# Performance work log

Measured on AMD Instinct MI355X. Metric: run time of the kernel, lower is better.

## Reference

```python
import jax, jax.numpy as jnp
import numpy as np

KERNELS = (7, 9, 11)   # kernel_sizes, dilation=1 each
HEADS_PER = 2          # num_head // len(kernel_sizes)
HEAD_DIM = 32          # dim // num_head
DIM = 192


def _win_idx(L, K):
    # NATTEN non-causal window start: centered, clamped to stay in-bounds.
    starts = jnp.clip(jnp.arange(L) - K // 2, 0, L - K)
    return starts[:, None] + jnp.arange(K)[None, :]  # [L, K]


def _na2d(q, k, v, K):
    # q,k,v: [B, h, H, W, D]; q pre-scaled. Neighborhood attention, kernel KxK.
    B, h, H, W, D = q.shape
    ih = _win_idx(H, K)  # [H, K]
    iw = _win_idx(W, K)  # [W, K]
    kr = k[:, :, ih]     # [B, h, H, Kh, W, D]  rows gathered once
    # loop over the Kw kernel taps (small fixed structural loop)
    attn = jnp.stack(
        [jnp.einsum('bnijd,bnikjd->bnijk', q, kr[:, :, :, :, iw[:, kw], :])
         for kw in range(K)], axis=-1)                 # [B,h,H,W,Kh,Kw]
    attn = jax.nn.softmax(attn.reshape(B, h, H, W, K * K), axis=-1)
    attn = attn.reshape(B, h, H, W, K, K)
    vr = v[:, :, ih]     # [B, h, H, Kh, W, D]
    y = jnp.zeros_like(q)
    for kw in range(K):
        y = y + jnp.einsum('bnijk,bnikjd->bnijd',
                           attn[..., kw], vr[:, :, :, :, iw[:, kw], :])
    return y             # [B, h, H, W, D]


def _forward(x, w_qkv, b_qkv, w_proj, b_proj):
    B, H, W, C = x.shape
    qkv = x @ w_qkv + b_qkv                      # [B,H,W,3*DIM]
    scale = HEAD_DIM ** -0.5
    outs = []
    off = 0
    for K in KERNELS:
        ch = 3 * HEADS_PER * HEAD_DIM            # 192 per scale
        xi = qkv[..., off:off + ch]
        off += ch
        r = xi.reshape(B, H, W, 3, HEADS_PER, HEAD_DIM)
        q = jnp.transpose(r[:, :, :, 0], (0, 3, 1, 2, 4)) * scale
        k = jnp.transpose(r[:, :, :, 1], (0, 3, 1, 2, 4))
        v = jnp.transpose(r[:, :, :, 2], (0, 3, 1, 2, 4))
        y = _na2d(q, k, v, K)                    # [B,h,H,W,D]
        outs.append(jnp.transpose(y, (0, 2, 3, 1, 4)).reshape(B, H, W, HEADS_PER * HEAD_DIM))
    out = jnp.concatenate(outs, axis=-1)         # [B,H,W,DIM]
    return out @ w_proj + b_proj


def setup_inputs() -> dict:
    key = jax.random.key(0)
    ks = jax.random.split(key, 4)
    x = jax.random.normal(ks[0], (4, 96, 96, DIM), jnp.float32)
    w_qkv = jax.random.normal(ks[1], (DIM, 3 * DIM), jnp.float32) * 0.02
    b_qkv = jnp.zeros((3 * DIM,), jnp.float32)
    w_proj = jax.random.normal(ks[2], (DIM, DIM), jnp.float32) * 0.02
    b_proj = jnp.zeros((DIM,), jnp.float32)
    return {'x': x, 'w_qkv': w_qkv, 'b_qkv': b_qkv, 'w_proj': w_proj, 'b_proj': b_proj}


def reference(x, w_qkv, b_qkv, w_proj, b_proj):
    return _forward(x, w_qkv, b_qkv, w_proj, b_proj)
```

## Files before the change

kernel.cpp:

```cpp
#include <hip/hip_runtime.h>
#include <cstddef>

constexpr int B_ = 4, H_ = 96, W_ = 96, C_ = 192, QKVC = 576;
constexpr int NPIX = B_ * H_ * W_;
constexpr float C2 = 0.25503486208385085f;

typedef __attribute__((ext_vector_type(8))) short bf16x8;
typedef __attribute__((ext_vector_type(4))) float f32x4;
typedef unsigned short ushort_t;

__device__ __forceinline__ unsigned short f2bf(float f) {
    unsigned int u = __builtin_bit_cast(unsigned int, f);
    u += 0x7fffu + ((u >> 16) & 1u);
    return (unsigned short)(u >> 16);
}
__device__ __forceinline__ float bf2f(unsigned short h) {
    unsigned int u = ((unsigned int)h) << 16;
    return __builtin_bit_cast(float, u);
}
__device__ __forceinline__ unsigned int pack2(unsigned short a, unsigned short b) {
    return (unsigned int)a | ((unsigned int)b << 16);
}
__device__ __forceinline__ float fexp2(float x) {
#if __has_builtin(__builtin_amdgcn_exp2f)
    return __builtin_amdgcn_exp2f(x);
#else
    return __expf(x * 0.6931471805599453f);
#endif
}

__global__ __launch_bounds__(256) void convert_x_kernel(
    const float* __restrict__ x, ushort_t* __restrict__ xh, int n4)
{
    int i = blockIdx.x * 256 + threadIdx.x;
    if (i >= n4) return;
    float4 v = ((const float4*)x)[i];
    uint2 p;
    p.x = pack2(f2bf(v.x), f2bf(v.y));
    p.y = pack2(f2bf(v.z), f2bf(v.w));
    ((uint2*)xh)[i] = p;
}

__global__ __launch_bounds__(256) void convert_w_kernel(
    const float* __restrict__ w_qkv, const float* __restrict__ w_proj,
    ushort_t* __restrict__ wqt, ushort_t* __restrict__ wpt_h,
    ushort_t* __restrict__ wpt_l)
{
    int idx = blockIdx.x * 256 + threadIdx.x;
    if (idx < 576 * 192) {
        int n = idx / 192, k = idx - n * 192;
        wqt[idx] = f2bf(w_qkv[(size_t)k * 576 + n]);
    } else {
        int i2 = idx - 576 * 192;
        if (i2 < 192 * 192) {
            int n = i2 / 192, k = i2 - n * 192;
            float v = w_proj[(size_t)k * 192 + n];
            unsigned short h = f2bf(v);
            wpt_h[i2] = h;
            wpt_l[i2] = f2bf(v - bf2f(h));
        }
    }
}

template<bool BSPLIT, bool OUTBF, bool VT, int NT>
__global__ __launch_bounds__(256) void gemm_mfma2_kernel(
    const ushort_t* __restrict__ A,
    const ushort_t* __restrict__ Bt_h, const ushort_t* __restrict__ Bt_l,
    const float* __restrict__ bias, void* __restrict__ Cout,
    ushort_t* __restrict__ vTout, int M, int N, int K)
{
    constexpr int NPB = BSPLIT ? 2 : 1;
    constexpr int NI = NT / 32;
    __shared__ __align__(16) ushort_t As[8 * 64 * 8];
    __shared__ __align__(16) ushort_t Bs[NPB][8 * NT * 8];

    const int tid = threadIdx.x;
    const int lane = tid & 63;
    const int w = tid >> 6;
    const int wm = (w & 1) * 32;
    const int wn = (w >> 1) * (NT / 2);
    const int fm = lane & 15;
    const int fq = lane >> 4;

    const int phys = blockIdx.x;
    const int bid = (phys & 7) * (int)(gridDim.x >> 3) + (phys >> 3);
    const int ntiles = N / NT;
    const int m0 = (bid / ntiles) * 64;
    const int n0 = (bid % ntiles) * NT;

    f32x4 acc[2][NI];
    #pragma unroll
    for (int mi = 0; mi < 2; ++mi)
        #pragma unroll
        for (int ni = 0; ni < NI; ++ni)
            acc[mi][ni] = (f32x4){0.f, 0.f, 0.f, 0.f};

    for (int k0 = 0; k0 < K; k0 += 64) {
        __syncthreads();
        #pragma unroll
        for (int it = 0; it < 2; ++it) {
            int idx = it * 256 + tid;
            int m = idx >> 3, kc = idx & 7;
            uint4 v = *(const uint4*)(A + (size_t)(m0 + m) * K + k0 + kc * 8);
            *(uint4*)(&As[0] + (kc * 64 + (m ^ kc)) * 8) = v;
        }
        #pragma unroll
        for (int it = 0; it < NI; ++it) {
            int idx = it * 256 + tid;
            int n = idx >> 3, kc = idx & 7;
            int phys_g = kc * NT + (n ^ kc);
            *(uint4*)(&Bs[0][0] + phys_g * 8) =
                *(const uint4*)(Bt_h + (size_t)(n0 + n) * K + k0 + kc * 8);
            if constexpr (BSPLIT)
                *(uint4*)(&Bs[NPB - 1][0] + phys_g * 8) =
                    *(const uint4*)(Bt_l + (size_t)(n0 + n) * K + k0 + kc * 8);
        }
        __syncthreads();

        #pragma unroll
        for (int kt2 = 0; kt2 < 2; ++kt2) {
            const int kc = kt2 * 4 + fq;
            bf16x8 ah[2], bh[NI];
            #pragma unroll
            for (int mi = 0; mi < 2; ++mi)
                ah[mi] = *(const bf16x8*)(&As[0] + (kc * 64 + ((wm + mi * 16 + fm) ^ kc)) * 8);
            #pragma unroll
            for (int ni = 0; ni < NI; ++ni)
                bh[ni] = *(const bf16x8*)(&Bs[0][0] + (kc * NT + ((wn + ni * 16 + fm) ^ kc)) * 8);
            #pragma unroll
            for (int mi = 0; mi < 2; ++mi)
                #pragma unroll
                for (int ni = 0; ni < NI; ++ni)
                    acc[mi][ni] = __builtin_amdgcn_mfma_f32_16x16x32_bf16(
                        ah[mi], bh[ni], acc[mi][ni], 0, 0, 0);
            if constexpr (BSPLIT) {
                bf16x8 bl[NI];
                #pragma unroll
                for (int ni = 0; ni < NI; ++ni)
                    bl[ni] = *(const bf16x8*)(&Bs[NPB - 1][0] + (kc * NT + ((wn + ni * 16 + fm) ^ kc)) * 8);
                #pragma unroll
                for (int mi = 0; mi < 2; ++mi)
                    #pragma unroll
                    for (int ni = 0; ni < NI; ++ni)
                        acc[mi][ni] = __builtin_amdgcn_mfma_f32_16x16x32_bf16(
                            ah[mi], bl[ni], acc[mi][ni], 0, 0, 0);
            }
        }
    }

    #pragma unroll
    for (int ni = 0; ni < NI; ++ni) {
        const int lcol = wn + ni * 16 + fm;
        const int col = n0 + lcol;
        const float bv = bias[col];
        const int vl = lcol - 128;
        #pragma unroll
        for (int mi = 0; mi < 2; ++mi) {
            const int rbase = m0 + wm + mi * 16 + fq * 4;
            if constexpr (VT) {
                if (vl >= 0) {
                    int bb = rbase / 9216;
                    int rem = rbase - bb * 9216;
                    int ii = rem / 96;
                    int jj = rem - ii * 96;
                    int hh = vl >> 5, dd = vl & 31;
                    unsigned long long pk =
                          (unsigned long long)f2bf(acc[mi][ni][0] + bv)
                        | ((unsigned long long)f2bf(acc[mi][ni][1] + bv) << 16)
                        | ((unsigned long long)f2bf(acc[mi][ni][2] + bv) << 32)
                        | ((unsigned long long)f2bf(acc[mi][ni][3] + bv) << 48);
                    *(unsigned long long*)(vTout
                        + ((size_t)((bb * 96 + ii) * 6) + (n0 / 192) * 2 + hh) * 3072
                        + (size_t)dd * 96 + jj) = pk;
                    continue;
                }
            }
            #pragma unroll
            for (int r = 0; r < 4; ++r) {
                float val = acc[mi][ni][r] + bv;
                if constexpr (OUTBF)
                    ((ushort_t*)Cout)[(size_t)(rbase + r) * N + col] = f2bf(val);
                else
                    ((float*)Cout)[(size_t)(rbase + r) * N + col] = val;
            }
        }
    }
}

__global__ __launch_bounds__(384, 5) void na2d_kernel(
    const ushort_t* __restrict__ qkv, const ushort_t* __restrict__ vT,
    ushort_t* __restrict__ attn)
{
    __shared__ ushort_t Kb[2][96 * 40];
    __shared__ ushort_t Vtb[2][32 * 104];
    __shared__ ushort_t Pb[6][16 * 40];

    int phys = blockIdx.x;
    int idx = (phys & 7) * 288 + (phys >> 3);

    const int g = idx % 3; idx /= 3;
    const int h = idx & 1; idx >>= 1;
    const int i = idx % 96;
    const int b = idx / 96;

    const int K = 7 + 2 * g, cc = K >> 1;
    int si = i - cc; if (si < 0) si = 0; if (si > H_ - K) si = H_ - K;

    const int tid = threadIdx.x;
    const int w = tid >> 6, lane = tid & 63;
    const int fm = lane & 15, fq = lane >> 4;
    const int pixbase = w * 16;

    int cb = (pixbase - cc) & ~7;
    if (cb < 0) cb = 0; if (cb > 64) cb = 64;
    const int col0 = cb + fm, col1 = cb + 16 + fm;

    float bm0[4], bm1[4];
    #pragma unroll
    for (int r = 0; r < 4; ++r) {
        int jj = pixbase + fq * 4 + r - cc;
        if (jj < 0) jj = 0; if (jj > W_ - K) jj = W_ - K;
        bm0[r] = ((unsigned)(col0 - jj) < (unsigned)K) ? 0.f : -1e30f;
        bm1[r] = ((unsigned)(col1 - jj) < (unsigned)K) ? 0.f : -1e30f;
    }

    const size_t rowstride = (size_t)W_ * QKVC;
    const bf16x8 qfrag = *(const bf16x8*)(
        qkv + (size_t)(b * H_ + i) * rowstride + (size_t)(pixbase + fm) * QKVC
        + g * 192 + h * 32 + fq * 8);

    const int scol = tid >> 2, sch = tid & 3;
    const size_t kgoff = (size_t)scol * QKVC + g * 192 + 64 + h * 32 + sch * 8;
    const int klds = scol * 40 + ((sch ^ (scol & 3)) << 3);
    const int vd = tid / 12, vc8 = tid - vd * 12;
    const int vlds = vd * 104 + vc8 * 8;
    const size_t vslice = ((size_t)((b * H_ + si) * 6) + g * 2 + h) * 3072;

    f32x4 y0 = {0.f, 0.f, 0.f, 0.f}, y1 = {0.f, 0.f, 0.f, 0.f};
    float lacc[4] = {0.f, 0.f, 0.f, 0.f};

    uint4 kv = *(const uint4*)(qkv + (size_t)(b * H_ + si) * rowstride + kgoff);
    uint4 vv = *(const uint4*)(vT + vslice + (size_t)tid * 8);

    for (int t = 0; t < K; ++t) {
        *(uint4*)&Kb[t & 1][klds] = kv;
        *(uint4*)&Vtb[t & 1][vlds] = vv;
        if (t + 1 < K) {
            kv = *(const uint4*)(qkv + (size_t)(b * H_ + si + t + 1) * rowstride + kgoff);
            vv = *(const uint4*)(vT + vslice + (size_t)(t + 1) * 18432 + (size_t)tid * 8);
        }
        __syncthreads();

        bf16x8 kf0 = *(const bf16x8*)&Kb[t & 1][col0 * 40 + ((fq ^ (col0 & 3)) << 3)];
        bf16x8 kf1 = *(const bf16x8*)&Kb[t & 1][col1 * 40 + ((fq ^ (col1 & 3)) << 3)];
        f32x4 s0 = __builtin_amdgcn_mfma_f32_16x16x32_bf16(
            qfrag, kf0, (f32x4){0.f, 0.f, 0.f, 0.f}, 0, 0, 0);
        f32x4 s1 = __builtin_amdgcn_mfma_f32_16x16x32_bf16(
            qfrag, kf1, (f32x4){0.f, 0.f, 0.f, 0.f}, 0, 0, 0);

        #pragma unroll
        for (int r = 0; r < 4; ++r) {
            float e0 = fexp2(fmaf(s0[r], C2, bm0[r]));
            float e1 = fexp2(fmaf(s1[r], C2, bm1[r]));
            unsigned short p0 = f2bf(e0), p1 = f2bf(e1);
            lacc[r] += bf2f(p0) + bf2f(p1);
            const int m = fq * 4 + r;
            Pb[w][m * 40 + (((fm >> 3) ^ (m & 3)) << 3) + (fm & 7)] = p0;
            Pb[w][m * 40 + ((((fm >> 3) + 2) ^ (m & 3)) << 3) + (fm & 7)] = p1;
        }

        bf16x8 pf = *(const bf16x8*)&Pb[w][fm * 40 + ((fq ^ (fm & 3)) << 3)];
        bf16x8 vf0 = *(const bf16x8*)&Vtb[t & 1][fm * 104 + cb + fq * 8];
        bf16x8 vf1 = *(const bf16x8*)&Vtb[t & 1][(16 + fm) * 104 + cb + fq * 8];
        y0 = __builtin_amdgcn_mfma_f32_16x16x32_bf16(pf, vf0, y0, 0, 0, 0);
        y1 = __builtin_amdgcn_mfma_f32_16x16x32_bf16(pf, vf1, y1, 0, 0, 0);
    }

    #pragma unroll
    for (int r = 0; r < 4; ++r) {
        float l = lacc[r];
        l += __shfl_xor(l, 1); l += __shfl_xor(l, 2);
        l += __shfl_xor(l, 4); l += __shfl_xor(l, 8);
        const float inv = 1.f / l;
        const int j = pixbase + fq * 4 + r;
        const size_t o = (size_t)((b * H_ + i) * W_ + j) * C_ + g * 64 + h * 32 + fm;
        attn[o]      = f2bf(y0[r] * inv);
        attn[o + 16] = f2bf(y1[r] * inv);
    }
}

extern "C" void kernel_launch(void* const* d_in, const int* in_sizes, int n_in,
                              void* d_out, int out_size, void* d_ws, size_t ws_size,
                              hipStream_t stream)
{
    const float* x      = (const float*)d_in[0];
    const float* w_qkv  = (const float*)d_in[1];
    const float* b_qkv  = (const float*)d_in[2];
    const float* w_proj = (const float*)d_in[3];
    const float* b_proj = (const float*)d_in[4];
    float* out = (float*)d_out;

    char* ws = (char*)d_ws;
    ushort_t* qkvh  = (ushort_t*)ws;
    char*     reg1  = ws + (size_t)NPIX * QKVC * 2;
    ushort_t* xh    = (ushort_t*)reg1;
    ushort_t* attn  = (ushort_t*)reg1;
    char*     wbase = reg1 + (size_t)NPIX * C_ * 2;
    ushort_t* wqt   = (ushort_t*)wbase;
    ushort_t* wpt_h = (ushort_t*)(wbase + 576 * 192 * 2);
    ushort_t* wpt_l = (ushort_t*)(wbase + 576 * 192 * 2 + 192 * 192 * 2);
    ushort_t* vT    = (ushort_t*)(wbase + 576 * 192 * 2 + 2 * 192 * 192 * 2);

    convert_x_kernel<<<(NPIX * C_ / 4 + 255) / 256, 256, 0, stream>>>(
        x, xh, NPIX * C_ / 4);
    convert_w_kernel<<<(576 * 192 + 192 * 192 + 255) / 256, 256, 0, stream>>>(
        w_qkv, w_proj, wqt, wpt_h, wpt_l);

    gemm_mfma2_kernel<false, true, true, 192><<<(NPIX / 64) * (QKVC / 192), 256, 0, stream>>>(
        xh, wqt, nullptr, b_qkv, qkvh, vT, NPIX, QKVC, C_);

    na2d_kernel<<<2304, 384, 0, stream>>>(qkvh, vT, attn);

    gemm_mfma2_kernel<true, false, false, 96><<<(NPIX / 64) * (C_ / 96), 256, 0, stream>>>(
        attn, wpt_h, wpt_l, b_proj, out, nullptr, NPIX, C_, C_);
}
```

Baseline: 161.1 us.

## Drop LDS staging in NA2D kernel; load K/V fragments directly into registers

The neighborhood-attention kernel no longer stages K, V and the probability tile through shared memory with __syncthreads. Each lane now loads its MFMA K and V fragments straight from global memory with register double-buffering. Swapping the QK^T operand order leaves the score tile in the layout needed for the PV MFMA, so P is packed in registers. Blocks shrink from 384 to 128 threads with three times as many blocks, which removes LDS traffic and barriers but adds redundant, less coalesced global loads that now rely on cache.

```diff
diff --git a/kernel.cpp b/kernel.cpp
--- a/kernel.cpp
+++ b/kernel.cpp
@@ -187,21 +187,18 @@
     }
 }
 
-__global__ __launch_bounds__(384, 5) void na2d_kernel(
+__global__ __launch_bounds__(128, 4) void na2d_kernel(
     const ushort_t* __restrict__ qkv, const ushort_t* __restrict__ vT,
     ushort_t* __restrict__ attn)
 {
-    __shared__ ushort_t Kb[2][96 * 40];
-    __shared__ ushort_t Vtb[2][32 * 104];
-    __shared__ ushort_t Pb[6][16 * 40];
-
     int phys = blockIdx.x;
-    int idx = (phys & 7) * 288 + (phys >> 3);
-
-    const int g = idx % 3; idx /= 3;
-    const int h = idx & 1; idx >>= 1;
-    const int i = idx % 96;
-    const int b = idx / 96;
+    int idx = (phys & 7) * 864 + (phys >> 3);
+
+    const int c2 = idx % 3; idx /= 3;
+    const int g  = idx % 3; idx /= 3;
+    const int h  = idx & 1; idx >>= 1;
+    const int i  = idx % 96;
+    const int b  = idx / 96;
 
     const int K = 7 + 2 * g, cc = K >> 1;
     int si = i - cc; if (si < 0) si = 0; if (si > H_ - K) si = H_ - K;
@@ -209,78 +206,84 @@
     const int tid = threadIdx.x;
     const int w = tid >> 6, lane = tid & 63;
     const int fm = lane & 15, fq = lane >> 4;
-    const int pixbase = w * 16;
+    const int pixbase = (c2 * 2 + w) * 16;
 
     int cb = (pixbase - cc) & ~7;
     if (cb < 0) cb = 0; if (cb > 64) cb = 64;
-    const int col0 = cb + fm, col1 = cb + 16 + fm;
-
-    float bm0[4], bm1[4];
+
+    const int jlane = pixbase + fm;
+    int sjl = jlane - cc; if (sjl < 0) sjl = 0; if (sjl > W_ - K) sjl = W_ - K;
+    float b0[4], b1[4];
     #pragma unroll
     for (int r = 0; r < 4; ++r) {
-        int jj = pixbase + fq * 4 + r - cc;
-        if (jj < 0) jj = 0; if (jj > W_ - K) jj = W_ - K;
-        bm0[r] = ((unsigned)(col0 - jj) < (unsigned)K) ? 0.f : -1e30f;
-        bm1[r] = ((unsigned)(col1 - jj) < (unsigned)K) ? 0.f : -1e30f;
+        b0[r] = ((unsigned)(cb + fq * 4 + r - sjl)      < (unsigned)K) ? 0.f : -1e30f;
+        b1[r] = ((unsigned)(cb + 16 + fq * 4 + r - sjl) < (unsigned)K) ? 0.f : -1e30f;
     }
 
     const size_t rowstride = (size_t)W_ * QKVC;
     const bf16x8 qfrag = *(const bf16x8*)(
-        qkv + (size_t)(b * H_ + i) * rowstride + (size_t)(pixbase + fm) * QKVC
+        qkv + (size_t)(b * H_ + i) * rowstride + (size_t)jlane * QKVC
         + g * 192 + h * 32 + fq * 8);
 
-    const int scol = tid >> 2, sch = tid & 3;
-    const size_t kgoff = (size_t)scol * QKVC + g * 192 + 64 + h * 32 + sch * 8;
-    const int klds = scol * 40 + ((sch ^ (scol & 3)) << 3);
-    const int vd = tid / 12, vc8 = tid - vd * 12;
-    const int vlds = vd * 104 + vc8 * 8;
+    const ushort_t* kp0 = qkv + (size_t)(b * H_ + si) * rowstride
+        + (size_t)(cb + fm) * QKVC + g * 192 + 64 + h * 32 + fq * 8;
+    const ushort_t* kp1 = kp0 + (size_t)16 * QKVC;
     const size_t vslice = ((size_t)((b * H_ + si) * 6) + g * 2 + h) * 3072;
+    const ushort_t* vp = vT + vslice + (size_t)fm * 96 + cb + fq * 4;
 
     f32x4 y0 = {0.f, 0.f, 0.f, 0.f}, y1 = {0.f, 0.f, 0.f, 0.f};
-    float lacc[4] = {0.f, 0.f, 0.f, 0.f};
-
-    uint4 kv = *(const uint4*)(qkv + (size_t)(b * H_ + si) * rowstride + kgoff);
-    uint4 vv = *(const uint4*)(vT + vslice + (size_t)tid * 8);
+    float lsum = 0.f;
+
+    bf16x8 kf0 = *(const bf16x8*)kp0;
+    bf16x8 kf1 = *(const bf16x8*)kp1;
+    uint2 va = *(const uint2*)(vp);
+    uint2 vb = *(const uint2*)(vp + 16);
+    uint2 vc = *(const uint2*)(vp + 1536);
+    uint2 vd = *(const uint2*)(vp + 1552);
 
     for (int t = 0; t < K; ++t) {
-        *(uint4*)&Kb[t & 1][klds] = kv;
-        *(uint4*)&Vtb[t & 1][vlds] = vv;
+        const bf16x8 ck0 = kf0, ck1 = kf1;
+        const bf16x8 cv0 = __builtin_bit_cast(bf16x8, (uint4){va.x, va.y, vb.x, vb.y});
+        const bf16x8 cv1 = __builtin_bit_cast(bf16x8, (uint4){vc.x, vc.y, vd.x, vd.y});
         if (t + 1 < K) {
-            kv = *(const uint4*)(qkv + (size_t)(b * H_ + si + t + 1) * rowstride + kgoff);
-            vv = *(const uint4*)(vT + vslice + (size_t)(t + 1) * 18432 + (size_t)tid * 8);
-        }
-        __syncthreads();
-
-        bf16x8 kf0 = *(const bf16x8*)&Kb[t & 1][col0 * 40 + ((fq ^ (col0 & 3)) << 3)];
-        bf16x8 kf1 = *(const bf16x8*)&Kb[t & 1][col1 * 40 + ((fq ^ (col1 & 3)) << 3)];
+            kp0 += rowstride; kp1 += rowstride; vp += 18432;
+            kf0 = *(const bf16x8*)kp0;
+            kf1 = *(const bf16x8*)kp1;
+            va = *(const uint2*)(vp);
+            vb = *(const uint2*)(vp + 16);
+            vc = *(const uint2*)(vp + 1536);
+            vd = *(const uint2*)(vp + 1552);
+        }
+
         f32x4 s0 = __builtin_amdgcn_mfma_f32_16x16x32_bf16(
-            qfrag, kf0, (f32x4){0.f, 0.f, 0.f, 0.f}, 0, 0, 0);
+            ck0, qfrag, (f32x4){0.f, 0.f, 0.f, 0.f}, 0, 0, 0);
         f32x4 s1 = __builtin_amdgcn_mfma_f32_16x16x32_bf16(
-            qfrag, kf1, (f32x4){0.f, 0.f, 0.f, 0.f}, 0, 0, 0);
-
-        #pragma unroll
-        for (int r = 0; r < 4; ++r) {
-            float e0 = fexp2(fmaf(s0[r], C2, bm0[r]));
-            float e1 = fexp2(fmaf(s1[r], C2, bm1[r]));
-            unsigned short p0 = f2bf(e0), p1 = f2bf(e1);
-            lacc[r] += bf2f(p0) + bf2f(p1);
-            const int m = fq * 4 + r;
-            Pb[w][m * 40 + (((fm >> 3) ^ (m & 3)) << 3) + (fm & 7)] = p0;
-            Pb[w][m * 40 + ((((fm >> 3) + 2) ^ (m & 3)) << 3) + (fm & 7)] = p1;
-        }
-
-        bf16x8 pf = *(const bf16x8*)&Pb[w][fm * 40 + ((fq ^ (fm & 3)) << 3)];
-        bf16x8 vf0 = *(const bf16x8*)&Vtb[t & 1][fm * 104 + cb + fq * 8];
-        bf16x8 vf1 = *(const bf16x8*)&Vtb[t & 1][(16 + fm) * 104 + cb + fq * 8];
-        y0 = __builtin_amdgcn_mfma_f32_16x16x32_bf16(pf, vf0, y0, 0, 0, 0);
-        y1 = __builtin_amdgcn_mfma_f32_16x16x32_bf16(pf, vf1, y1, 0, 0, 0);
-    }
+            ck1, qfrag, (f32x4){0.f, 0.f, 0.f, 0.f}, 0, 0, 0);
+
+        unsigned short p00 = f2bf(fexp2(fmaf(s0[0], C2, b0[0])));
+        unsigned short p01 = f2bf(fexp2(fmaf(s0[1], C2, b0[1])));
+        unsigned short p02 = f2bf(fexp2(fmaf(s0[2], C2, b0[2])));
+        unsigned short p03 = f2bf(fexp2(fmaf(s0[3], C2, b0[3])));
+        unsigned short p10 = f2bf(fexp2(fmaf(s1[0], C2, b1[0])));
+        unsigned short p11 = f2bf(fexp2(fmaf(s1[1], C2, b1[1])));
+        unsigned short p12 = f2bf(fexp2(fmaf(s1[2], C2, b1[2])));
+        unsigned short p13 = f2bf(fexp2(fmaf(s1[3], C2, b1[3])));
+        lsum += (bf2f(p00) + bf2f(p01)) + (bf2f(p02) + bf2f(p03))
+              + (bf2f(p10) + bf2f(p11)) + (bf2f(p12) + bf2f(p13));
+        const bf16x8 pa = __builtin_bit_cast(bf16x8, (uint4){
+            pack2(p00, p01), pack2(p02, p03),
+            pack2(p10, p11), pack2(p12, p13)});
+
+        y0 = __builtin_amdgcn_mfma_f32_16x16x32_bf16(pa, cv0, y0, 0, 0, 0);
+        y1 = __builtin_amdgcn_mfma_f32_16x16x32_bf16(pa, cv1, y1, 0, 0, 0);
+    }
+
+    lsum += __shfl_xor(lsum, 16);
+    lsum += __shfl_xor(lsum, 32);
 
     #pragma unroll
     for (int r = 0; r < 4; ++r) {
-        float l = lacc[r];
-        l += __shfl_xor(l, 1); l += __shfl_xor(l, 2);
-        l += __shfl_xor(l, 4); l += __shfl_xor(l, 8);
+        const float l = __shfl(lsum, fq * 4 + r);
         const float inv = 1.f / l;
         const int j = pixbase + fq * 4 + r;
         const size_t o = (size_t)((b * H_ + i) * W_ + j) * C_ + g * 64 + h * 32 + fm;
@@ -319,7 +322,7 @@
     gemm_mfma2_kernel<false, true, true, 192><<<(NPIX / 64) * (QKVC / 192), 256, 0, stream>>>(
         xh, wqt, nullptr, b_qkv, qkvh, vT, NPIX, QKVC, C_);
 
-    na2d_kernel<<<2304, 384, 0, stream>>>(qkvh, vT, attn);
+    na2d_kernel<<<6912, 128, 0, stream>>>(qkvh, vT, attn);
 
     gemm_mfma2_kernel<true, false, false, 96><<<(NPIX / 64) * (C_ / 96), 256, 0, stream>>>(
         attn, wpt_h, wpt_l, b_proj, out, nullptr, NPIX, C_, C_);
```

Result: slower. 184.6 us (+14.6%).

## Compute transposed scores so P feeds PV MFMA directly from registers

Applied to the files above, without the earlier changes.

Swaps the MFMA operands for the QK^T product so each lane holds the scores for its own pixel. The exponentiated probabilities can then be packed straight into the A operand of the PV MFMA, with V loaded in a matching permuted k-order. This removes the per-wave shared-memory P buffer, its scattered stores and reloads, and shrinks the row-sum reduction. The risk is that the permuted V reads are narrower (uint2), which may add LDS instructions or bank conflicts.

```diff
diff --git a/kernel.cpp b/kernel.cpp
--- a/kernel.cpp
+++ b/kernel.cpp
@@ -193,7 +193,6 @@
 {
     __shared__ ushort_t Kb[2][96 * 40];
     __shared__ ushort_t Vtb[2][32 * 104];
-    __shared__ ushort_t Pb[6][16 * 40];
 
     int phys = blockIdx.x;
     int idx = (phys & 7) * 288 + (phys >> 3);
@@ -215,18 +214,18 @@
     if (cb < 0) cb = 0; if (cb > 64) cb = 64;
     const int col0 = cb + fm, col1 = cb + 16 + fm;
 
-    float bm0[4], bm1[4];
+    const int jlane = pixbase + fm;
+    int sjl = jlane - cc; if (sjl < 0) sjl = 0; if (sjl > W_ - K) sjl = W_ - K;
+    float b0[4], b1[4];
     #pragma unroll
     for (int r = 0; r < 4; ++r) {
-        int jj = pixbase + fq * 4 + r - cc;
-        if (jj < 0) jj = 0; if (jj > W_ - K) jj = W_ - K;
-        bm0[r] = ((unsigned)(col0 - jj) < (unsigned)K) ? 0.f : -1e30f;
-        bm1[r] = ((unsigned)(col1 - jj) < (unsigned)K) ? 0.f : -1e30f;
+        b0[r] = ((unsigned)(cb + fq * 4 + r - sjl)      < (unsigned)K) ? 0.f : -1e30f;
+        b1[r] = ((unsigned)(cb + 16 + fq * 4 + r - sjl) < (unsigned)K) ? 0.f : -1e30f;
     }
 
     const size_t rowstride = (size_t)W_ * QKVC;
     const bf16x8 qfrag = *(const bf16x8*)(
-        qkv + (size_t)(b * H_ + i) * rowstride + (size_t)(pixbase + fm) * QKVC
+        qkv + (size_t)(b * H_ + i) * rowstride + (size_t)jlane * QKVC
         + g * 192 + h * 32 + fq * 8);
 
     const int scol = tid >> 2, sch = tid & 3;
@@ -237,7 +236,7 @@
     const size_t vslice = ((size_t)((b * H_ + si) * 6) + g * 2 + h) * 3072;
 
     f32x4 y0 = {0.f, 0.f, 0.f, 0.f}, y1 = {0.f, 0.f, 0.f, 0.f};
-    float lacc[4] = {0.f, 0.f, 0.f, 0.f};
+    float lsum = 0.f;
 
     uint4 kv = *(const uint4*)(qkv + (size_t)(b * H_ + si) * rowstride + kgoff);
     uint4 vv = *(const uint4*)(vT + vslice + (size_t)tid * 8);
@@ -253,34 +252,44 @@
 
         bf16x8 kf0 = *(const bf16x8*)&Kb[t & 1][col0 * 40 + ((fq ^ (col0 & 3)) << 3)];
         bf16x8 kf1 = *(const bf16x8*)&Kb[t & 1][col1 * 40 + ((fq ^ (col1 & 3)) << 3)];
+        const ushort_t* vb0 = &Vtb[t & 1][fm * 104 + cb + fq * 4];
+        const ushort_t* vb1 = &Vtb[t & 1][(16 + fm) * 104 + cb + fq * 4];
+        uint2 va0 = *(const uint2*)(vb0);
+        uint2 va1 = *(const uint2*)(vb0 + 16);
+        uint2 va2 = *(const uint2*)(vb1);
+        uint2 va3 = *(const uint2*)(vb1 + 16);
+        const bf16x8 cv0 = __builtin_bit_cast(bf16x8, (uint4){va0.x, va0.y, va1.x, va1.y});
+        const bf16x8 cv1 = __builtin_bit_cast(bf16x8, (uint4){va2.x, va2.y, va3.x, va3.y});
+
         f32x4 s0 = __builtin_amdgcn_mfma_f32_16x16x32_bf16(
-            qfrag, kf0, (f32x4){0.f, 0.f, 0.f, 0.f}, 0, 0, 0);
+            kf0, qfrag, (f32x4){0.f, 0.f, 0.f, 0.f}, 0, 0, 0);
         f32x4 s1 = __builtin_amdgcn_mfma_f32_16x16x32_bf16(
-            qfrag, kf1, (f32x4){0.f, 0.f, 0.f, 0.f}, 0, 0, 0);
-
-        #pragma unroll
-        for (int r = 0; r < 4; ++r) {
-            float e0 = fexp2(fmaf(s0[r], C2, bm0[r]));
-            float e1 = fexp2(fmaf(s1[r], C2, bm1[r]));
-            unsigned short p0 = f2bf(e0), p1 = f2bf(e1);
-            lacc[r] += bf2f(p0) + bf2f(p1);
-            const int m = fq * 4 + r;
-            Pb[w][m * 40 + (((fm >> 3) ^ (m & 3)) << 3) + (fm & 7)] = p0;
-            Pb[w][m * 40 + ((((fm >> 3) + 2) ^ (m & 3)) << 3) + (fm & 7)] = p1;
-        }
-
-        bf16x8 pf = *(const bf16x8*)&Pb[w][fm * 40 + ((fq ^ (fm & 3)) << 3)];
-        bf16x8 vf0 = *(const bf16x8*)&Vtb[t & 1][fm * 104 + cb + fq * 8];
-        bf16x8 vf1 = *(const bf16x8*)&Vtb[t & 1][(16 + fm) * 104 + cb + fq * 8];
-        y0 = __builtin_amdgcn_mfma_f32_16x16x32_bf16(pf, vf0, y0, 0, 0, 0);
-        y1 = __builtin_amdgcn_mfma_f32_16x16x32_bf16(pf, vf1, y1, 0, 0, 0);
-    }
+            kf1, qfrag, (f32x4){0.f, 0.f, 0.f, 0.f}, 0, 0, 0);
+
+        unsigned short p00 = f2bf(fexp2(fmaf(s0[0], C2, b0[0])));
+        unsigned short p01 = f2bf(fexp2(fmaf(s0[1], C2, b0[1])));
+        unsigned short p02 = f2bf(fexp2(fmaf(s0[2], C2, b0[2])));
+        unsigned short p03 = f2bf(fexp2(fmaf(s0[3], C2, b0[3])));
+        unsigned short p10 = f2bf(fexp2(fmaf(s1[0], C2, b1[0])));
+        unsigned short p11 = f2bf(fexp2(fmaf(s1[1], C2, b1[1])));
+        unsigned short p12 = f2bf(fexp2(fmaf(s1[2], C2, b1[2])));
+        unsigned short p13 = f2bf(fexp2(fmaf(s1[3], C2, b1[3])));
+        lsum += (bf2f(p00) + bf2f(p01)) + (bf2f(p02) + bf2f(p03))
+              + (bf2f(p10) + bf2f(p11)) + (bf2f(p12) + bf2f(p13));
+        const bf16x8 pa = __builtin_bit_cast(bf16x8, (uint4){
+            pack2(p00, p01), pack2(p02, p03),
+            pack2(p10, p11), pack2(p12, p13)});
+
+        y0 = __builtin_amdgcn_mfma_f32_16x16x32_bf16(pa, cv0, y0, 0, 0, 0);
+        y1 = __builtin_amdgcn_mfma_f32_16x16x32_bf16(pa, cv1, y1, 0, 0, 0);
+    }
+
+    lsum += __shfl_xor(lsum, 16);
+    lsum += __shfl_xor(lsum, 32);
 
     #pragma unroll
     for (int r = 0; r < 4; ++r) {
-        float l = lacc[r];
-        l += __shfl_xor(l, 1); l += __shfl_xor(l, 2);
-        l += __shfl_xor(l, 4); l += __shfl_xor(l, 8);
+        const float l = __shfl(lsum, fq * 4 + r);
         const float inv = 1.f / l;
         const int j = pixbase + fq * 4 + r;
         const size_t o = (size_t)((b * H_ + i) * W_ + j) * C_ + g * 64 + h * 32 + fm;
```

Result: faster. 155.5 us (-3.5%).
